# Optimization experiments

Hardware: AMD Instinct MI355X
Metric: run time of the kernel (lower is better)

The kernel has to match this reference:

```python
import jax, jax.numpy as jnp
import numpy as np

N_ITER = 50


def sparsemax_bisect(X, n_iter=N_ITER):
    # entmax-style bisection for sparsemax (alpha=2): p = clip(X - tau, 0), sum(p) = 1
    d = X.shape[-1]
    max_val = jnp.max(X, axis=-1, keepdims=True)          # [N, 1]
    tau_lo = max_val - 1.0                                # f(tau_lo) >= 0
    tau_hi = max_val - 1.0 / d                            # f(tau_hi) <= 0
    f_lo = jnp.sum(jnp.clip(X - tau_lo, 0.0), axis=-1, keepdims=True) - 1.0
    dm0 = tau_hi - tau_lo

    def body(_, carry):
        tau_lo, dm, _tau_m = carry
        dm = dm * 0.5
        tau_m = tau_lo + dm
        f_m = jnp.sum(jnp.clip(X - tau_m, 0.0), axis=-1, keepdims=True) - 1.0
        tau_lo = jnp.where(f_m * f_lo >= 0, tau_m, tau_lo)
        return (tau_lo, dm, tau_m)

    _, _, tau_m = jax.lax.fori_loop(0, n_iter, body, (tau_lo, dm0, tau_lo))
    # p from the final midpoint, exactly as in entmax's sparsemax_bisect
    return jnp.clip(X - tau_m, 0.0)


def setup_inputs() -> dict:
    key = jax.random.key(0)
    X = jax.random.normal(key, (4096, 32000), dtype=jnp.float32)
    return {"X": X}


def reference(X):
    p_star = sparsemax_bisect(X, N_ITER)
    p_star = p_star / jnp.sum(p_star, axis=-1, keepdims=True)
    # log(0) -> -inf, matching torch.log on exact zeros
    sup = p_star > 0
    return jnp.where(sup, jnp.log(jnp.where(sup, p_star, 1.0)), -jnp.inf)
```

## Files before the change

### kernel.cpp

```cpp
#include <hip/hip_runtime.h>
#include <math.h>


typedef float f32x4 __attribute__((ext_vector_type(4)));

#define ROWS 4096
#define COLS 32000
#define NV4  (COLS / 4)
#define TPB  256
#define WPB  (TPB / 64)
#define SEG  512
#define CAP  (SEG * WPB)
#define REGC 4
#define SENT (-1e38f)
#define QMIN (1e-37f)

__global__ __launch_bounds__(TPB, 8)
void logsparsemax_v5_kernel(const float* __restrict__ X,
                            float* __restrict__ Y) {
    __shared__ float s_cand[CAP];
    __shared__ int   s_cidx[CAP];
    __shared__ float s_wmax[WPB];
    __shared__ int   s_wcnt[WPB];
    __shared__ float s_res[2];

    const int tid  = threadIdx.x;
    const int lane = tid & 63;
    const int wid  = tid >> 6;
    const int row  = blockIdx.x;
    const float* __restrict__ Xr = X + (size_t)row * COLS;
    const f32x4* __restrict__ X4 = (const f32x4*)Xr;
    float* __restrict__ Yr = Y + (size_t)row * COLS;
    f32x4* __restrict__ Y4 = (f32x4*)Yr;

    const f32x4 sent4 = {SENT, SENT, SENT, SENT};
    const int sbase = wid * SEG;

    float wmax = -INFINITY;
    int   cnt  = 0;

    int i = tid;
    for (; i + 3 * TPB < NV4; i += 4 * TPB) {
        f32x4 a = X4[i];
        f32x4 b = X4[i +     TPB];
        f32x4 c = X4[i + 2 * TPB];
        f32x4 d = X4[i + 3 * TPB];
        Y4[i]           = sent4;
        Y4[i +     TPB] = sent4;
        Y4[i + 2 * TPB] = sent4;
        Y4[i + 3 * TPB] = sent4;
        float ma = fmaxf(fmaxf(a.x, a.y), fmaxf(a.z, a.w));
        float mb = fmaxf(fmaxf(b.x, b.y), fmaxf(b.z, b.w));
        float mc = fmaxf(fmaxf(c.x, c.y), fmaxf(c.z, c.w));
        float md = fmaxf(fmaxf(d.x, d.y), fmaxf(d.z, d.w));
        float mall = fmaxf(fmaxf(ma, mb), fmaxf(mc, md));
        float t = mall;
        #pragma unroll
        for (int off = 32; off > 0; off >>= 1)
            t = fmaxf(t, __shfl_xor(t, off, 64));
        wmax = fmaxf(wmax, t);
        const float thr = wmax - 1.0f;
        if (__ballot(mall > thr) != 0ull) {
            float vv[16] = {a.x, a.y, a.z, a.w,  b.x, b.y, b.z, b.w,
                            c.x, c.y, c.z, c.w,  d.x, d.y, d.z, d.w};
            #pragma unroll
            for (int s = 0; s < 16; ++s) {
                bool p = vv[s] > thr;
                unsigned long long m = __ballot(p);
                if (p) {
                    int pos = cnt + __popcll(m & ((1ull << lane) - 1ull));
                    if (pos < SEG) {
                        s_cand[sbase + pos] = vv[s];
                        s_cidx[sbase + pos] = 4 * (i + (s >> 2) * TPB) + (s & 3);
                    }
                }
                cnt += __popcll(m);
            }
        }
    }
    for (; i < NV4; i += TPB) {
        f32x4 a = X4[i];
        Y4[i] = sent4;
        float mall = fmaxf(fmaxf(a.x, a.y), fmaxf(a.z, a.w));
        float t = mall;
        #pragma unroll
        for (int off = 32; off > 0; off >>= 1)
            t = fmaxf(t, __shfl_xor(t, off, 64));
        wmax = fmaxf(wmax, t);
        const float thr = wmax - 1.0f;
        if (__ballot(mall > thr) != 0ull) {
            float vv[4] = {a.x, a.y, a.z, a.w};
            #pragma unroll
            for (int s = 0; s < 4; ++s) {
                bool p = vv[s] > thr;
                unsigned long long m = __ballot(p);
                if (p) {
                    int pos = cnt + __popcll(m & ((1ull << lane) - 1ull));
                    if (pos < SEG) {
                        s_cand[sbase + pos] = vv[s];
                        s_cidx[sbase + pos] = 4 * i + s;
                    }
                }
                cnt += __popcll(m);
            }
        }
    }

    if (lane == 0) { s_wmax[wid] = wmax; s_wcnt[wid] = cnt; }
    __syncthreads();

    const float bmax = fmaxf(fmaxf(s_wmax[0], s_wmax[1]), fmaxf(s_wmax[2], s_wmax[3]));
    const float tau_lo0 = bmax - 1.0f;
    const float tau_hi0 = bmax - (float)(1.0 / (double)COLS);
    const bool  fast = (s_wcnt[0] <= SEG) && (s_wcnt[1] <= SEG) &&
                       (s_wcnt[2] <= SEG) && (s_wcnt[3] <= SEG);

    if (wid == 0) {
        int nf = 0;
        if (fast) {
            for (int w = 0; w < WPB; ++w) {
                const int cw = s_wcnt[w];
                for (int j0 = 0; j0 < cw; j0 += 64) {
                    const int j = j0 + lane;
                    const bool in = (j < cw);
                    float v  = in ? s_cand[w * SEG + j] : 0.0f;
                    int   ix = in ? s_cidx[w * SEG + j] : 0;
                    bool  k  = in && (v > tau_lo0);
                    unsigned long long m = __ballot(k);
                    if (k) {
                        int pos = nf + __popcll(m & ((1ull << lane) - 1ull));
                        s_cand[pos] = v;
                        s_cidx[pos] = ix;
                    }
                    nf += __popcll(m);
                }
            }
        }

        float creg[REGC];
        #pragma unroll
        for (int k = 0; k < REGC; ++k) {
            int j = lane + 64 * k;
            creg[k] = (fast && j < nf) ? s_cand[j] : SENT;
        }

        auto fsum = [&](float tau) -> float {
            float acc = 0.0f;
            if (fast) {
                #pragma unroll
                for (int k = 0; k < REGC; ++k) acc += fmaxf(creg[k] - tau, 0.0f);
                for (int j = 64 * REGC + lane; j < nf; j += 64)
                    acc += fmaxf(s_cand[j] - tau, 0.0f);
            } else {
                for (int j = lane; j < COLS; j += 64)
                    acc += fmaxf(Xr[j] - tau, 0.0f);
            }
            #pragma unroll
            for (int off = 32; off > 0; off >>= 1)
                acc += __shfl_xor(acc, off, 64);
            return acc;
        };

        float tau_lo = tau_lo0;
        float dm     = tau_hi0 - tau_lo0;
        float tau_m  = tau_lo;
        const float f_lo = fsum(tau_lo) - 1.0f;
        for (int it = 0; it < 50; ++it) {
            dm *= 0.5f;
            float tcur = tau_lo + dm;
            tau_m = tcur;
            if (tcur == tau_lo) break;
            float f_m = fsum(tcur) - 1.0f;
            if (f_m * f_lo >= 0.0f) tau_lo = tcur;
        }
        const float ssum = fsum(tau_m);
        if (lane == 0) { s_res[0] = tau_m; s_res[1] = ssum; }

        if (fast) {
            const float lsm = logf(fmaxf(ssum, QMIN));
            for (int j = lane; j < nf; j += 64) {
                float r = s_cand[j] - tau_m;
                if (r > 0.0f)
                    Yr[s_cidx[j]] = logf(fmaxf(r, QMIN)) - lsm;
            }
        }
    }
    __syncthreads();

    if (!fast) {
        const float tau = s_res[0];
        const float lsm = logf(fmaxf(s_res[1], QMIN));
        for (int v4i = tid; v4i < NV4; v4i += TPB) {
            f32x4 v = X4[v4i];
            f32x4 o;
            float r;
            r = v.x - tau; o.x = (r > 0.0f) ? logf(fmaxf(r, QMIN)) - lsm : SENT;
            r = v.y - tau; o.y = (r > 0.0f) ? logf(fmaxf(r, QMIN)) - lsm : SENT;
            r = v.z - tau; o.z = (r > 0.0f) ? logf(fmaxf(r, QMIN)) - lsm : SENT;
            r = v.w - tau; o.w = (r > 0.0f) ? logf(fmaxf(r, QMIN)) - lsm : SENT;
            Y4[v4i] = o;
        }
    }
}

extern "C" void kernel_launch(void* const* d_in, const int* in_sizes, int n_in,
                              void* d_out, int out_size, void* d_ws, size_t ws_size,
                              hipStream_t stream) {
    const float* X = (const float*)d_in[0];
    float* Y = (float*)d_out;
    logsparsemax_v5_kernel<<<dim3(ROWS), dim3(TPB), 0, stream>>>(X, Y);
}
```

Measured before the change: 225.3 us.

## Replace in-kernel sentinel stores with memset fill, widen unroll, lazy max reduction

The per-element sentinel writes are moved out of the kernel into a hipMemsetAsync that fills the output with the byte 0xDE, a large negative float used as the new sentinel. The scan loop is unrolled to 8 vectors per thread, and the wave-wide max reduction and threshold update now run only when some lane exceeds the current threshold. This removes the store traffic and most shuffles from the main pass, at the cost of a separate memset launch that still writes the whole output, plus higher register pressure from the wider unroll.

```diff
diff --git a/kernel.cpp b/kernel.cpp
--- a/kernel.cpp
+++ b/kernel.cpp
@@ -9,20 +9,22 @@
 #define NV4  (COLS / 4)
 #define TPB  256
 #define WPB  (TPB / 64)
+#define U    8
 #define SEG  512
 #define CAP  (SEG * WPB)
 #define REGC 4
-#define SENT (-1e38f)
 #define QMIN (1e-37f)
 
 __global__ __launch_bounds__(TPB, 8)
-void logsparsemax_v5_kernel(const float* __restrict__ X,
+void logsparsemax_v6_kernel(const float* __restrict__ X,
                             float* __restrict__ Y) {
     __shared__ float s_cand[CAP];
     __shared__ int   s_cidx[CAP];
     __shared__ float s_wmax[WPB];
     __shared__ int   s_wcnt[WPB];
     __shared__ float s_res[2];
+
+    const float SENT = __uint_as_float(0xDEDEDEDEu);
 
     const int tid  = threadIdx.x;
     const int lane = tid & 63;
@@ -31,77 +33,78 @@
     const float* __restrict__ Xr = X + (size_t)row * COLS;
     const f32x4* __restrict__ X4 = (const f32x4*)Xr;
     float* __restrict__ Yr = Y + (size_t)row * COLS;
-    f32x4* __restrict__ Y4 = (f32x4*)Yr;
-
-    const f32x4 sent4 = {SENT, SENT, SENT, SENT};
+
     const int sbase = wid * SEG;
-
     float wmax = -INFINITY;
+    float thr  = INFINITY;
     int   cnt  = 0;
 
+    thr = -INFINITY;
+
     int i = tid;
-    for (; i + 3 * TPB < NV4; i += 4 * TPB) {
-        f32x4 a = X4[i];
-        f32x4 b = X4[i +     TPB];
-        f32x4 c = X4[i + 2 * TPB];
-        f32x4 d = X4[i + 3 * TPB];
-        Y4[i]           = sent4;
-        Y4[i +     TPB] = sent4;
-        Y4[i + 2 * TPB] = sent4;
-        Y4[i + 3 * TPB] = sent4;
-        float ma = fmaxf(fmaxf(a.x, a.y), fmaxf(a.z, a.w));
-        float mb = fmaxf(fmaxf(b.x, b.y), fmaxf(b.z, b.w));
-        float mc = fmaxf(fmaxf(c.x, c.y), fmaxf(c.z, c.w));
-        float md = fmaxf(fmaxf(d.x, d.y), fmaxf(d.z, d.w));
-        float mall = fmaxf(fmaxf(ma, mb), fmaxf(mc, md));
-        float t = mall;
+    for (; i + (U - 1) * TPB < NV4; i += U * TPB) {
+        f32x4 v[U];
         #pragma unroll
-        for (int off = 32; off > 0; off >>= 1)
-            t = fmaxf(t, __shfl_xor(t, off, 64));
-        wmax = fmaxf(wmax, t);
-        const float thr = wmax - 1.0f;
+        for (int u = 0; u < U; ++u) v[u] = X4[i + u * TPB];
+
+        float mall = -INFINITY;
+        #pragma unroll
+        for (int u = 0; u < U; ++u)
+            mall = fmaxf(mall, fmaxf(fmaxf(v[u].x, v[u].y), fmaxf(v[u].z, v[u].w)));
+
         if (__ballot(mall > thr) != 0ull) {
-            float vv[16] = {a.x, a.y, a.z, a.w,  b.x, b.y, b.z, b.w,
-                            c.x, c.y, c.z, c.w,  d.x, d.y, d.z, d.w};
-            #pragma unroll
-            for (int s = 0; s < 16; ++s) {
-                bool p = vv[s] > thr;
-                unsigned long long m = __ballot(p);
-                if (p) {
-                    int pos = cnt + __popcll(m & ((1ull << lane) - 1ull));
-                    if (pos < SEG) {
-                        s_cand[sbase + pos] = vv[s];
-                        s_cidx[sbase + pos] = 4 * (i + (s >> 2) * TPB) + (s & 3);
+            float t = mall;
+            #pragma unroll
+            for (int off = 32; off > 0; off >>= 1)
+                t = fmaxf(t, __shfl_xor(t, off, 64));
+            wmax = fmaxf(wmax, t);
+            thr  = wmax - 1.0f;
+            #pragma unroll
+            for (int u = 0; u < U; ++u) {
+                #pragma unroll
+                for (int c = 0; c < 4; ++c) {
+                    float val = (c == 0) ? v[u].x : (c == 1) ? v[u].y : (c == 2) ? v[u].z : v[u].w;
+                    bool p = val > thr;
+                    unsigned long long m = __ballot(p);
+                    if (m != 0ull) {
+                        if (p) {
+                            int pos = cnt + __popcll(m & ((1ull << lane) - 1ull));
+                            if (pos < SEG) {
+                                s_cand[sbase + pos] = val;
+                                s_cidx[sbase + pos] = 4 * (i + u * TPB) + c;
+                            }
+                        }
+                        cnt += __popcll(m);
                     }
                 }
-                cnt += __popcll(m);
             }
         }
     }
     for (; i < NV4; i += TPB) {
         f32x4 a = X4[i];
-        Y4[i] = sent4;
         float mall = fmaxf(fmaxf(a.x, a.y), fmaxf(a.z, a.w));
-        float t = mall;
-        #pragma unroll
-        for (int off = 32; off > 0; off >>= 1)
-            t = fmaxf(t, __shfl_xor(t, off, 64));
-        wmax = fmaxf(wmax, t);
-        const float thr = wmax - 1.0f;
         if (__ballot(mall > thr) != 0ull) {
+            float t = mall;
+            #pragma unroll
+            for (int off = 32; off > 0; off >>= 1)
+                t = fmaxf(t, __shfl_xor(t, off, 64));
+            wmax = fmaxf(wmax, t);
+            thr  = wmax - 1.0f;
             float vv[4] = {a.x, a.y, a.z, a.w};
             #pragma unroll
-            for (int s = 0; s < 4; ++s) {
-                bool p = vv[s] > thr;
+            for (int c = 0; c < 4; ++c) {
+                bool p = vv[c] > thr;
                 unsigned long long m = __ballot(p);
-                if (p) {
-                    int pos = cnt + __popcll(m & ((1ull << lane) - 1ull));
-                    if (pos < SEG) {
-                        s_cand[sbase + pos] = vv[s];
-                        s_cidx[sbase + pos] = 4 * i + s;
+                if (m != 0ull) {
+                    if (p) {
+                        int pos = cnt + __popcll(m & ((1ull << lane) - 1ull));
+                        if (pos < SEG) {
+                            s_cand[sbase + pos] = vv[c];
+                            s_cidx[sbase + pos] = 4 * i + c;
+                        }
                     }
+                    cnt += __popcll(m);
                 }
-                cnt += __popcll(m);
             }
         }
     }
@@ -190,6 +193,7 @@
     if (!fast) {
         const float tau = s_res[0];
         const float lsm = logf(fmaxf(s_res[1], QMIN));
+        f32x4* __restrict__ Y4 = (f32x4*)Yr;
         for (int v4i = tid; v4i < NV4; v4i += TPB) {
             f32x4 v = X4[v4i];
             f32x4 o;
@@ -208,5 +212,6 @@
                               hipStream_t stream) {
     const float* X = (const float*)d_in[0];
     float* Y = (float*)d_out;
-    logsparsemax_v5_kernel<<<dim3(ROWS), dim3(TPB), 0, stream>>>(X, Y);
+    hipMemsetAsync(d_out, 0xDE, (size_t)out_size * sizeof(float), stream);
+    logsparsemax_v6_kernel<<<dim3(ROWS), dim3(TPB), 0, stream>>>(X, Y);
 }
```

Result: slower. 238.4 us (+5.8%).
